# Kernel tuning notes

Measured on AMD Instinct MI355X. Metric: run time of the kernel, lower is better.

The kernel has to match this reference:

```python
import jax, jax.numpy as jnp
import numpy as np

B, H, W, C = 32, 64, 64, 192
WS, SHIFT, NH = 8, 4, 6
HID = int(C * 2.0)
N = WS * WS
HD = C // NH
SCALE = HD ** -0.5


def _rel_index():
    coords = np.stack(np.meshgrid(np.arange(WS), np.arange(WS), indexing='ij')).reshape(2, -1)
    rel = (coords[:, :, None] - coords[:, None, :]).transpose(1, 2, 0)
    rel[:, :, 0] += WS - 1
    rel[:, :, 1] += WS - 1
    rel[:, :, 0] *= 2 * WS - 1
    return rel.sum(-1)  # [N, N] int


def _attn_mask():
    img = np.zeros((H, W))
    cnt = 0
    sl = (slice(0, -WS), slice(-WS, -SHIFT), slice(-SHIFT, None))
    for hs in sl:
        for ws_ in sl:
            img[hs, ws_] = cnt
            cnt += 1
    mw = img.reshape(H // WS, WS, W // WS, WS).transpose(0, 2, 1, 3).reshape(-1, N)
    am = mw[:, None, :] - mw[:, :, None]  # unsqueeze(1) - unsqueeze(2)
    return np.where(am != 0, -100.0, 0.0).astype(np.float32)  # [nW, N, N]

REL_IDX = jnp.asarray(_rel_index())
ATTN_MASK = jnp.asarray(_attn_mask())


def _ln(x, g, b, eps=1e-5):
    m = jnp.mean(x, -1, keepdims=True)
    v = jnp.mean((x - m) ** 2, -1, keepdims=True)
    return (x - m) * jax.lax.rsqrt(v + eps) * g + b


def setup_inputs() -> dict:
    key = jax.random.key(0)
    ks = jax.random.split(key, 16)
    s = 0.02
    return {
        'x': jax.random.normal(ks[0], (B, H, W, C), jnp.float32),
        'norm1_g': jnp.ones((C,), jnp.float32),
        'norm1_b': jnp.zeros((C,), jnp.float32),
        'qkv_w': jax.random.normal(ks[1], (C, 3 * C), jnp.float32) * s,
        'qkv_b': jnp.zeros((3 * C,), jnp.float32),
        'proj_w': jax.random.normal(ks[2], (C, C), jnp.float32) * s,
        'proj_b': jnp.zeros((C,), jnp.float32),
        'rel_bias_table': jax.random.normal(ks[3], ((2 * WS - 1) ** 2, NH), jnp.float32) * s,
        'norm2_g': jnp.ones((C,), jnp.float32),
        'norm2_b': jnp.zeros((C,), jnp.float32),
        'mlp_w1': jax.random.normal(ks[4], (C, HID), jnp.float32) * s,
        'mlp_b1': jnp.zeros((HID,), jnp.float32),
        'mlp_w2': jax.random.normal(ks[5], (HID, C), jnp.float32) * s,
        'mlp_b2': jnp.zeros((C,), jnp.float32),
    }


def reference(x, norm1_g, norm1_b, qkv_w, qkv_b, proj_w, proj_b, rel_bias_table,
              norm2_g, norm2_b, mlp_w1, mlp_b1, mlp_w2, mlp_b2):
    nWh, nWw = H // WS, W // WS
    nW = nWh * nWw
    shortcut = x
    h = _ln(x, norm1_g, norm1_b)
    # cyclic shift
    h = jnp.roll(h, shift=(-SHIFT, -SHIFT), axis=(1, 2))
    # window partition -> [B*nW, N, C]
    hw = h.reshape(B, nWh, WS, nWw, WS, C).transpose(0, 1, 3, 2, 4, 5).reshape(B * nW, N, C)
    # qkv
    qkv = hw @ qkv_w + qkv_b  # [B_, N, 3C]
    qkv = qkv.reshape(B * nW, N, 3, NH, HD).transpose(2, 0, 3, 1, 4)
    q, k, v = qkv[0], qkv[1], qkv[2]  # [B_, NH, N, HD]
    attn = jnp.einsum('bhnd,bhmd->bhnm', q * SCALE, k)
    # relative position bias: [NH, N, N]
    bias = rel_bias_table[REL_IDX.reshape(-1)].reshape(N, N, NH).transpose(2, 0, 1)
    attn = attn + bias[None]
    # shift mask
    attn = attn.reshape(B, nW, NH, N, N) + ATTN_MASK[None, :, None]
    attn = jax.nn.softmax(attn.reshape(B * nW, NH, N, N), axis=-1)
    out = jnp.einsum('bhnm,bhmd->bhnd', attn, v).transpose(0, 2, 1, 3).reshape(B * nW, N, C)
    out = out @ proj_w + proj_b
    # window reverse
    out = out.reshape(B, nWh, nWw, WS, WS, C).transpose(0, 1, 3, 2, 4, 5).reshape(B, H, W, C)
    out = jnp.roll(out, shift=(SHIFT, SHIFT), axis=(1, 2))
    h = shortcut + out
    # MLP
    m = _ln(h, norm2_g, norm2_b)
    m = jax.nn.gelu(m @ mlp_w1 + mlp_b1, approximate=False) @ mlp_w2 + mlp_b2
    return h + m
```

## Files before the change

### kernel.cpp

```cpp
#include <hip/hip_runtime.h>
#include <hip/hip_bf16.h>

#define CC 192

typedef __attribute__((ext_vector_type(8))) short bf16x8;
typedef __attribute__((ext_vector_type(4))) float f32x4;

__device__ __forceinline__ unsigned short f2bf(float f) {
    unsigned int u = __float_as_uint(f);
    u = (u + 0x7fffu + ((u >> 16) & 1u)) >> 16;
    return (unsigned short)u;
}

__device__ __forceinline__ f32x4 mfma16(bf16x8 a, bf16x8 b, f32x4 c) {
    return __builtin_amdgcn_mfma_f32_16x16x32_bf16(a, b, c, 0, 0, 0);
}

__global__ void k_prep(const float* __restrict__ qkv_w, const float* __restrict__ proj_w,
                       const float* __restrict__ w1, const float* __restrict__ w2,
                       const float* __restrict__ relTab,
                       unsigned short* __restrict__ qkvT, unsigned short* __restrict__ projT,
                       unsigned short* __restrict__ w1T, unsigned short* __restrict__ w2T,
                       float* __restrict__ biasT) {
    int idx = blockIdx.x * blockDim.x + threadIdx.x;
    if (idx < 110592) { int n = idx / 192, k = idx % 192; qkvT[idx] = f2bf(qkv_w[k * 576 + n]); return; }
    idx -= 110592;
    if (idx < 36864)  { int n = idx / 192, k = idx % 192; projT[idx] = f2bf(proj_w[k * 192 + n]); return; }
    idx -= 36864;
    if (idx < 73728)  { int n = idx / 192, k = idx % 192; w1T[idx] = f2bf(w1[k * 384 + n]); return; }
    idx -= 73728;
    if (idx < 73728)  { int n = idx / 384, k = idx % 384; w2T[idx] = f2bf(w2[k * 192 + n]); return; }
    idx -= 73728;
    if (idx < 24576) {
        int h = idx >> 12, i = (idx >> 6) & 63, j = idx & 63;
        int yi = i >> 3, xi = i & 7, yj = j >> 3, xj = j & 7;
        int rel = (yi - yj + 7) * 15 + (xi - xj + 7);
        biasT[idx] = relTab[rel * 6 + h];
    }
}

__global__ __launch_bounds__(768, 3) void k_fused(
    const float* __restrict__ x,
    const float* __restrict__ n1g, const float* __restrict__ n1b,
    const unsigned short* __restrict__ qkvT, const float* __restrict__ qkv_b,
    const unsigned short* __restrict__ projT, const float* __restrict__ proj_b,
    const float* __restrict__ biasTab,
    const float* __restrict__ n2g, const float* __restrict__ n2b,
    const unsigned short* __restrict__ w1T, const float* __restrict__ b1,
    const unsigned short* __restrict__ w2T, const float* __restrict__ b2,
    float* __restrict__ out)
{
    __shared__ __align__(16) char smem[73728];
    __shared__ int sOpos[64];
    char* const rA = smem;
    char* const rQ = smem + 24576;
    char* const rK = smem + 49152;
    char* const rG = smem + 24576;

    const int tid = threadIdx.x;
    const int wid = blockIdx.x;
    const int b = wid >> 6;
    const int win = wid & 63;
    const int wh = win >> 3, ww = win & 7;
    const int lane = tid & 63;
    const int wave = tid >> 6;
    const int lhi = lane >> 4, llo = lane & 15;

    if (tid < 512) {
        const int tok = tid >> 3;
        const int ch0 = (tid & 7) * 24;
        const int yi = tok >> 3, xi = tok & 7;
        const int oy = (wh * 8 + yi + 4) & 63;
        const int ox = (ww * 8 + xi + 4) & 63;
        const int base = ((b * 64 + oy) * 64 + ox) * CC;
        if ((tid & 7) == 0) sOpos[tok] = base;
        float v[24];
        float s = 0.f, ss = 0.f;
        #pragma unroll
        for (int i = 0; i < 6; ++i) {
            const float4 f = *(const float4*)(x + base + ch0 + i * 4);
            v[i*4+0]=f.x; v[i*4+1]=f.y; v[i*4+2]=f.z; v[i*4+3]=f.w;
            s  += f.x + f.y + f.z + f.w;
            ss += f.x*f.x + f.y*f.y + f.z*f.z + f.w*f.w;
        }
        s  += __shfl_xor(s, 1);  s  += __shfl_xor(s, 2);  s  += __shfl_xor(s, 4);
        ss += __shfl_xor(ss, 1); ss += __shfl_xor(ss, 2); ss += __shfl_xor(ss, 4);
        const float mean = s * (1.f / 192.f);
        const float rstd = rsqrtf(ss * (1.f / 192.f) - mean * mean + 1e-5f);
        char* aBase = rA + tok * 384;
        const int sw = (tok & 7) << 4;
        #pragma unroll
        for (int i = 0; i < 12; ++i) {
            const int c = ch0 + i * 2;
            const float a0 = (v[i*2+0] - mean) * rstd * n1g[c]   + n1b[c];
            const float a1 = (v[i*2+1] - mean) * rstd * n1g[c+1] + n1b[c+1];
            *(unsigned int*)(aBase + ((c * 2) ^ sw)) =
                (unsigned int)f2bf(a0) | ((unsigned int)f2bf(a1) << 16);
        }
    }
    __syncthreads();

    {
        const int cbase = wave * 48;
        f32x4 acc[4][3] = {};
        #pragma unroll
        for (int ks = 0; ks < 6; ++ks) {
            bf16x8 af[4];
            const int kbyte = ks * 64 + lhi * 16;
            #pragma unroll
            for (int m = 0; m < 4; ++m) {
                const int row = m * 16 + llo;
                af[m] = *(const bf16x8*)(rA + row * 384 + (kbyte ^ ((row & 7) << 4)));
            }
            #pragma unroll
            for (int n = 0; n < 3; ++n) {
                const int col = cbase + n * 16 + llo;
                const bf16x8 bfr = *(const bf16x8*)(qkvT + col * 192 + ks * 32 + lhi * 8);
                #pragma unroll
                for (int m = 0; m < 4; ++m) acc[m][n] = mfma16(af[m], bfr, acc[m][n]);
            }
        }
        __syncthreads();
        #pragma unroll
        for (int n = 0; n < 3; ++n) {
            const int c0 = cbase + n * 16;
            const int which = c0 / 192;
            const int rem = c0 - which * 192;
            const int h = rem >> 5;
            const int d = (rem & 31) + llo;
            const float bia = qkv_b[c0 + llo];
            #pragma unroll
            for (int m = 0; m < 4; ++m) {
                #pragma unroll
                for (int r = 0; r < 4; ++r) {
                    const int row = m * 16 + lhi * 4 + r;
                    if (which == 0)
                        *(unsigned short*)(rQ + h * 4096 + row * 64 + ((2 * d) ^ ((row & 3) << 4)))
                            = f2bf((acc[m][n][r] + bia) * 0.17677669529663687f);
                    else if (which == 1)
                        *(unsigned short*)(rK + h * 4096 + row * 64 + ((2 * d) ^ ((row & 3) << 4)))
                            = f2bf(acc[m][n][r] + bia);
                    else
                        *(unsigned short*)(rA + h * 4096 + d * 128 + ((2 * row) ^ ((d & 7) << 4)))
                            = f2bf(acc[m][n][r] + bia);
                }
            }
        }
    }
    __syncthreads();

    const int h = wave >> 1;
    const int mh = wave & 1;
    f32x4 pacc[2][2] = {};
    float rinv[2][4];
    {
        bf16x8 qf[2], kf[4];
        #pragma unroll
        for (int m = 0; m < 2; ++m) {
            const int t = (mh * 2 + m) * 16 + llo;
            qf[m] = *(const bf16x8*)(rQ + h * 4096 + t * 64 + ((lhi * 16) ^ ((t & 3) << 4)));
        }
        #pragma unroll
        for (int n = 0; n < 4; ++n) {
            const int t = n * 16 + llo;
            kf[n] = *(const bf16x8*)(rK + h * 4096 + t * 64 + ((lhi * 16) ^ ((t & 3) << 4)));
        }
        __syncthreads();

        f32x4 sacc[2][4] = {};
        #pragma unroll
        for (int m = 0; m < 2; ++m)
            #pragma unroll
            for (int n = 0; n < 4; ++n)
                sacc[m][n] = mfma16(qf[m], kf[n], sacc[m][n]);

        const bool eH = (wh == 7), eW = (ww == 7);
        int idj[4];
        #pragma unroll
        for (int n = 0; n < 4; ++n) {
            const int j = n * 16 + llo;
            idj[n] = (eH ? ((j >> 3) >= 4 ? 2 : 1) : 0) * 3 + (eW ? ((j & 7) >= 4 ? 2 : 1) : 0);
        }
        const float* bT = biasTab + h * 4096;
        #pragma unroll
        for (int m = 0; m < 2; ++m) {
            #pragma unroll
            for (int r = 0; r < 4; ++r) {
                const int i = (mh * 2 + m) * 16 + lhi * 4 + r;
                const int idi = (eH ? ((i >> 3) >= 4 ? 2 : 1) : 0) * 3 +
                                (eW ? ((i & 7) >= 4 ? 2 : 1) : 0);
                float sum = 0.f;
                unsigned short pb[4];
                #pragma unroll
                for (int n = 0; n < 4; ++n) {
                    const int j = n * 16 + llo;
                    float e = __expf(sacc[m][n][r] + bT[i * 64 + j]);
                    if (idi != idj[n]) e = 0.f;
                    sum += e;
                    pb[n] = f2bf(e);
                }
                sum += __shfl_xor(sum, 1);
                sum += __shfl_xor(sum, 2);
                sum += __shfl_xor(sum, 4);
                sum += __shfl_xor(sum, 8);
                rinv[m][r] = 1.f / sum;
                #pragma unroll
                for (int n = 0; n < 4; ++n) {
                    const int j = n * 16 + llo;
                    *(unsigned short*)(rQ + h * 8192 + i * 128 + ((2 * j) ^ ((i & 7) << 4))) = pb[n];
                }
            }
        }
        #pragma unroll
        for (int ks = 0; ks < 2; ++ks) {
            bf16x8 pf[2];
            #pragma unroll
            for (int m = 0; m < 2; ++m) {
                const int t = (mh * 2 + m) * 16 + llo;
                pf[m] = *(const bf16x8*)(rQ + h * 8192 + t * 128 + ((ks * 64 + lhi * 16) ^ ((t & 7) << 4)));
            }
            #pragma unroll
            for (int n = 0; n < 2; ++n) {
                const int d = n * 16 + llo;
                const bf16x8 vf = *(const bf16x8*)(rA + h * 4096 + d * 128 + ((ks * 64 + lhi * 16) ^ ((d & 7) << 4)));
                #pragma unroll
                for (int m = 0; m < 2; ++m) pacc[m][n] = mfma16(pf[m], vf, pacc[m][n]);
            }
        }
    }
    __syncthreads();
    {
        #pragma unroll
        for (int m = 0; m < 2; ++m) {
            #pragma unroll
            for (int n = 0; n < 2; ++n) {
                const int c = h * 32 + n * 16 + llo;
                #pragma unroll
                for (int r = 0; r < 4; ++r) {
                    const int i = (mh * 2 + m) * 16 + lhi * 4 + r;
                    *(unsigned short*)(rA + i * 384 + ((c * 2) ^ ((i & 7) << 4)))
                        = f2bf(pacc[m][n][r] * rinv[m][r]);
                }
            }
        }
    }
    __syncthreads();

    {
        const int cbase = wave * 16;
        f32x4 acc[4] = {};
        #pragma unroll
        for (int ks = 0; ks < 6; ++ks) {
            bf16x8 af[4];
            const int kbyte = ks * 64 + lhi * 16;
            #pragma unroll
            for (int m = 0; m < 4; ++m) {
                const int row = m * 16 + llo;
                af[m] = *(const bf16x8*)(rA + row * 384 + (kbyte ^ ((row & 7) << 4)));
            }
            const int col = cbase + llo;
            const bf16x8 bfr = *(const bf16x8*)(projT + col * 192 + ks * 32 + lhi * 8);
            #pragma unroll
            for (int m = 0; m < 4; ++m) acc[m] = mfma16(af[m], bfr, acc[m]);
        }
        const int c = cbase + llo;
        const float pb = proj_b[c];
        #pragma unroll
        for (int m = 0; m < 4; ++m) {
            #pragma unroll
            for (int r = 0; r < 4; ++r) {
                const int i = m * 16 + lhi * 4 + r;
                const int base = sOpos[i];
                out[base + c] = x[base + c] + acc[m][r] + pb;
            }
        }
    }
    __syncthreads();

    if (tid < 512) {
        const int tok = tid >> 3;
        const int ch0 = (tid & 7) * 24;
        const float* hp = out + sOpos[tok];
        float v[24]; float s = 0.f, ss = 0.f;
        #pragma unroll
        for (int i = 0; i < 6; ++i) {
            const float4 f = *(const float4*)(hp + ch0 + i * 4);
            v[i*4]=f.x; v[i*4+1]=f.y; v[i*4+2]=f.z; v[i*4+3]=f.w;
            s += f.x + f.y + f.z + f.w;
            ss += f.x*f.x + f.y*f.y + f.z*f.z + f.w*f.w;
        }
        s  += __shfl_xor(s, 1);  s  += __shfl_xor(s, 2);  s  += __shfl_xor(s, 4);
        ss += __shfl_xor(ss, 1); ss += __shfl_xor(ss, 2); ss += __shfl_xor(ss, 4);
        const float mean = s * (1.f / 192.f);
        const float rstd = rsqrtf(ss * (1.f / 192.f) - mean * mean + 1e-5f);
        char* aBase = rA + tok * 384;
        const int sw = (tok & 7) << 4;
        #pragma unroll
        for (int i = 0; i < 12; ++i) {
            const int c = ch0 + i * 2;
            const float a0 = (v[i*2]   - mean) * rstd * n2g[c]   + n2b[c];
            const float a1 = (v[i*2+1] - mean) * rstd * n2g[c+1] + n2b[c+1];
            *(unsigned int*)(aBase + ((c * 2) ^ sw)) =
                (unsigned int)f2bf(a0) | ((unsigned int)f2bf(a1) << 16);
        }
    }
    __syncthreads();

    {
        const int cbase = wave * 32;
        f32x4 acc[4][2] = {};
        #pragma unroll
        for (int ks = 0; ks < 6; ++ks) {
            bf16x8 af[4];
            const int kbyte = ks * 64 + lhi * 16;
            #pragma unroll
            for (int m = 0; m < 4; ++m) {
                const int row = m * 16 + llo;
                af[m] = *(const bf16x8*)(rA + row * 384 + (kbyte ^ ((row & 7) << 4)));
            }
            #pragma unroll
            for (int n = 0; n < 2; ++n) {
                const int col = cbase + n * 16 + llo;
                const bf16x8 bfr = *(const bf16x8*)(w1T + col * 192 + ks * 32 + lhi * 8);
                #pragma unroll
                for (int m = 0; m < 4; ++m) acc[m][n] = mfma16(af[m], bfr, acc[m][n]);
            }
        }
        #pragma unroll
        for (int n = 0; n < 2; ++n) {
            const int c = cbase + n * 16 + llo;
            const float bb = b1[c];
            #pragma unroll
            for (int m = 0; m < 4; ++m) {
                #pragma unroll
                for (int r = 0; r < 4; ++r) {
                    const int i = m * 16 + lhi * 4 + r;
                    const float u = acc[m][n][r] + bb;
                    const float g = 0.5f * u * (1.f + erff(u * 0.70710678118654752f));
                    *(unsigned short*)(rG + i * 768 + ((c * 2) ^ ((i & 7) << 4))) = f2bf(g);
                }
            }
        }
    }
    __syncthreads();

    {
        const int cbase = wave * 16;
        f32x4 acc[4] = {};
        #pragma unroll
        for (int ks = 0; ks < 12; ++ks) {
            bf16x8 af[4];
            const int kbyte = ks * 64 + lhi * 16;
            #pragma unroll
            for (int m = 0; m < 4; ++m) {
                const int row = m * 16 + llo;
                af[m] = *(const bf16x8*)(rG + row * 768 + (kbyte ^ ((row & 7) << 4)));
            }
            const int col = cbase + llo;
            const bf16x8 bfr = *(const bf16x8*)(w2T + col * 384 + ks * 32 + lhi * 8);
            #pragma unroll
            for (int m = 0; m < 4; ++m) acc[m] = mfma16(af[m], bfr, acc[m]);
        }
        const int c = cbase + llo;
        const float bb = b2[c];
        #pragma unroll
        for (int m = 0; m < 4; ++m) {
            #pragma unroll
            for (int r = 0; r < 4; ++r) {
                const int i = m * 16 + lhi * 4 + r;
                float* p = out + sOpos[i] + c;
                *p = *p + acc[m][r] + bb;
            }
        }
    }
}

extern "C" void kernel_launch(void* const* d_in, const int* in_sizes, int n_in,
                              void* d_out, int out_size, void* d_ws, size_t ws_size,
                              hipStream_t stream)
{
    const float* x      = (const float*)d_in[0];
    const float* n1g    = (const float*)d_in[1];
    const float* n1b    = (const float*)d_in[2];
    const float* qkv_w  = (const float*)d_in[3];
    const float* qkv_b  = (const float*)d_in[4];
    const float* proj_w = (const float*)d_in[5];
    const float* proj_b = (const float*)d_in[6];
    const float* relTab = (const float*)d_in[7];
    const float* n2g    = (const float*)d_in[8];
    const float* n2b    = (const float*)d_in[9];
    const float* w1     = (const float*)d_in[10];
    const float* b1     = (const float*)d_in[11];
    const float* w2     = (const float*)d_in[12];
    const float* b2     = (const float*)d_in[13];
    float* out = (float*)d_out;

    char* ws = (char*)d_ws;
    unsigned short* qkvT  = (unsigned short*)(ws);
    unsigned short* projT = (unsigned short*)(ws + 221184);
    unsigned short* w1T   = (unsigned short*)(ws + 294912);
    unsigned short* w2T   = (unsigned short*)(ws + 442368);
    float*          biasT = (float*)(ws + 589824);

    k_prep<<<1248, 256, 0, stream>>>(qkv_w, proj_w, w1, w2, relTab, qkvT, projT, w1T, w2T, biasT);
    k_fused<<<2048, 768, 0, stream>>>(x, n1g, n1b, qkvT, qkv_b, projT, proj_b, biasT,
                                      n2g, n2b, w1T, b1, w2T, b2, out);
}
```

Measured before the change: 297.0 us.

## Shrink fused Swin block LDS footprint to fit more workgroups per CU

Reorganizes shared-memory use in the fused Swin block kernel so the footprint drops from 72KB to 60KB. V is now staged in two halves, and the MLP is split into two hidden-column chunks that reuse a smaller GELU buffer. The QKV GEMM work is redistributed so each wave holds its own Q/K tile and a slice of V. Launch bounds are raised to 6 blocks per CU to target higher occupancy and better latency hiding. The cost is extra __syncthreads barriers, more live accumulators (accV held across attention) and higher register pressure under the tighter bound.

```diff
diff --git a/kernel.cpp b/kernel.cpp
--- a/kernel.cpp
+++ b/kernel.cpp
@@ -39,7 +39,7 @@
     }
 }
 
-__global__ __launch_bounds__(768, 3) void k_fused(
+__global__ __launch_bounds__(768, 6) void k_fused(
     const float* __restrict__ x,
     const float* __restrict__ n1g, const float* __restrict__ n1b,
     const unsigned short* __restrict__ qkvT, const float* __restrict__ qkv_b,
@@ -50,12 +50,8 @@
     const unsigned short* __restrict__ w2T, const float* __restrict__ b2,
     float* __restrict__ out)
 {
-    __shared__ __align__(16) char smem[73728];
+    __shared__ __align__(16) char smem[61440];
     __shared__ int sOpos[64];
-    char* const rA = smem;
-    char* const rQ = smem + 24576;
-    char* const rK = smem + 49152;
-    char* const rG = smem + 24576;
 
     const int tid = threadIdx.x;
     const int wid = blockIdx.x;
@@ -87,7 +83,7 @@
         ss += __shfl_xor(ss, 1); ss += __shfl_xor(ss, 2); ss += __shfl_xor(ss, 4);
         const float mean = s * (1.f / 192.f);
         const float rstd = rsqrtf(ss * (1.f / 192.f) - mean * mean + 1e-5f);
-        char* aBase = rA + tok * 384;
+        char* aBase = smem + tok * 384;
         const int sw = (tok & 7) << 4;
         #pragma unroll
         for (int i = 0; i < 12; ++i) {
@@ -100,9 +96,12 @@
     }
     __syncthreads();
 
-    {
-        const int cbase = wave * 48;
-        f32x4 acc[4][3] = {};
+    const int w = wave;
+    f32x4 accQK[4][2] = {};
+    f32x4 accV[4] = {};
+    {
+        const int cb = 32 * w;
+        const int cv = 384 + 16 * w;
         #pragma unroll
         for (int ks = 0; ks < 6; ++ks) {
             bf16x8 af[4];
@@ -110,47 +109,55 @@
             #pragma unroll
             for (int m = 0; m < 4; ++m) {
                 const int row = m * 16 + llo;
-                af[m] = *(const bf16x8*)(rA + row * 384 + (kbyte ^ ((row & 7) << 4)));
-            }
-            #pragma unroll
-            for (int n = 0; n < 3; ++n) {
-                const int col = cbase + n * 16 + llo;
-                const bf16x8 bfr = *(const bf16x8*)(qkvT + col * 192 + ks * 32 + lhi * 8);
-                #pragma unroll
-                for (int m = 0; m < 4; ++m) acc[m][n] = mfma16(af[m], bfr, acc[m][n]);
-            }
-        }
-        __syncthreads();
-        #pragma unroll
-        for (int n = 0; n < 3; ++n) {
-            const int c0 = cbase + n * 16;
-            const int which = c0 / 192;
-            const int rem = c0 - which * 192;
-            const int h = rem >> 5;
-            const int d = (rem & 31) + llo;
-            const float bia = qkv_b[c0 + llo];
+                af[m] = *(const bf16x8*)(smem + row * 384 + (kbyte ^ ((row & 7) << 4)));
+            }
+            #pragma unroll
+            for (int n = 0; n < 2; ++n) {
+                const bf16x8 bfr = *(const bf16x8*)(qkvT + (cb + n * 16 + llo) * 192 + ks * 32 + lhi * 8);
+                #pragma unroll
+                for (int m = 0; m < 4; ++m) accQK[m][n] = mfma16(af[m], bfr, accQK[m][n]);
+            }
+            const bf16x8 bfv = *(const bf16x8*)(qkvT + (cv + llo) * 192 + ks * 32 + lhi * 8);
+            #pragma unroll
+            for (int m = 0; m < 4; ++m) accV[m] = mfma16(af[m], bfv, accV[m]);
+        }
+    }
+    __syncthreads();
+
+    {
+        const bool isK = (w >= 6);
+        char* const dst = smem + (isK ? 36864 + (w - 6) * 4096 : 12288 + w * 4096);
+        #pragma unroll
+        for (int n = 0; n < 2; ++n) {
+            const int d = n * 16 + llo;
+            const float bia = qkv_b[32 * w + n * 16 + llo];
             #pragma unroll
             for (int m = 0; m < 4; ++m) {
                 #pragma unroll
                 for (int r = 0; r < 4; ++r) {
                     const int row = m * 16 + lhi * 4 + r;
-                    if (which == 0)
-                        *(unsigned short*)(rQ + h * 4096 + row * 64 + ((2 * d) ^ ((row & 3) << 4)))
-                            = f2bf((acc[m][n][r] + bia) * 0.17677669529663687f);
-                    else if (which == 1)
-                        *(unsigned short*)(rK + h * 4096 + row * 64 + ((2 * d) ^ ((row & 3) << 4)))
-                            = f2bf(acc[m][n][r] + bia);
-                    else
-                        *(unsigned short*)(rA + h * 4096 + d * 128 + ((2 * row) ^ ((d & 7) << 4)))
-                            = f2bf(acc[m][n][r] + bia);
-                }
-            }
-        }
-    }
-    __syncthreads();
-
-    const int h = wave >> 1;
-    const int mh = wave & 1;
+                    float vv = accQK[m][n][r] + bia;
+                    if (!isK) vv *= 0.17677669529663687f;
+                    *(unsigned short*)(dst + row * 64 + ((2 * d) ^ ((row & 3) << 4))) = f2bf(vv);
+                }
+            }
+        }
+        const float bv = qkv_b[384 + 16 * w + llo];
+        const int dl = (w & 1) * 16 + llo;
+        char* const vdst = smem + (w >> 1) * 2048;
+        #pragma unroll
+        for (int m = 0; m < 2; ++m) {
+            #pragma unroll
+            for (int r = 0; r < 4; ++r) {
+                const int k = m * 16 + lhi * 4 + r;
+                *(unsigned short*)(vdst + dl * 64 + ((2 * k) ^ ((dl & 3) << 4))) = f2bf(accV[m][r] + bv);
+            }
+        }
+    }
+    __syncthreads();
+
+    const int h = w >> 1;
+    const int mh = w & 1;
     f32x4 pacc[2][2] = {};
     float rinv[2][4];
     {
@@ -158,12 +165,12 @@
         #pragma unroll
         for (int m = 0; m < 2; ++m) {
             const int t = (mh * 2 + m) * 16 + llo;
-            qf[m] = *(const bf16x8*)(rQ + h * 4096 + t * 64 + ((lhi * 16) ^ ((t & 3) << 4)));
+            qf[m] = *(const bf16x8*)(smem + 12288 + h * 4096 + t * 64 + ((lhi * 16) ^ ((t & 3) << 4)));
         }
         #pragma unroll
         for (int n = 0; n < 4; ++n) {
             const int t = n * 16 + llo;
-            kf[n] = *(const bf16x8*)(rK + h * 4096 + t * 64 + ((lhi * 16) ^ ((t & 3) << 4)));
+            kf[n] = *(const bf16x8*)(smem + 36864 + h * 4096 + t * 64 + ((lhi * 16) ^ ((t & 3) << 4)));
         }
         __syncthreads();
 
@@ -207,25 +214,54 @@
                 #pragma unroll
                 for (int n = 0; n < 4; ++n) {
                     const int j = n * 16 + llo;
-                    *(unsigned short*)(rQ + h * 8192 + i * 128 + ((2 * j) ^ ((i & 7) << 4))) = pb[n];
-                }
-            }
-        }
-        #pragma unroll
-        for (int ks = 0; ks < 2; ++ks) {
+                    *(unsigned short*)(smem + 12288 + h * 8192 + i * 128 + ((2 * j) ^ ((i & 7) << 4))) = pb[n];
+                }
+            }
+        }
+        {
             bf16x8 pf[2];
             #pragma unroll
             for (int m = 0; m < 2; ++m) {
                 const int t = (mh * 2 + m) * 16 + llo;
-                pf[m] = *(const bf16x8*)(rQ + h * 8192 + t * 128 + ((ks * 64 + lhi * 16) ^ ((t & 7) << 4)));
+                pf[m] = *(const bf16x8*)(smem + 12288 + h * 8192 + t * 128 + ((lhi * 16) ^ ((t & 7) << 4)));
             }
             #pragma unroll
             for (int n = 0; n < 2; ++n) {
                 const int d = n * 16 + llo;
-                const bf16x8 vf = *(const bf16x8*)(rA + h * 4096 + d * 128 + ((ks * 64 + lhi * 16) ^ ((d & 7) << 4)));
+                const bf16x8 vf = *(const bf16x8*)(smem + h * 2048 + d * 64 + ((lhi * 16) ^ ((d & 3) << 4)));
                 #pragma unroll
                 for (int m = 0; m < 2; ++m) pacc[m][n] = mfma16(pf[m], vf, pacc[m][n]);
             }
+        }
+    }
+    __syncthreads();
+    {
+        const float bv = qkv_b[384 + 16 * w + llo];
+        const int dl = (w & 1) * 16 + llo;
+        char* const vdst = smem + (w >> 1) * 2048;
+        #pragma unroll
+        for (int m = 0; m < 2; ++m) {
+            #pragma unroll
+            for (int r = 0; r < 4; ++r) {
+                const int k = m * 16 + lhi * 4 + r;
+                *(unsigned short*)(vdst + dl * 64 + ((2 * k) ^ ((dl & 3) << 4))) = f2bf(accV[m + 2][r] + bv);
+            }
+        }
+    }
+    __syncthreads();
+    {
+        bf16x8 pf[2];
+        #pragma unroll
+        for (int m = 0; m < 2; ++m) {
+            const int t = (mh * 2 + m) * 16 + llo;
+            pf[m] = *(const bf16x8*)(smem + 12288 + h * 8192 + t * 128 + ((64 + lhi * 16) ^ ((t & 7) << 4)));
+        }
+        #pragma unroll
+        for (int n = 0; n < 2; ++n) {
+            const int d = n * 16 + llo;
+            const bf16x8 vf = *(const bf16x8*)(smem + h * 2048 + d * 64 + ((lhi * 16) ^ ((d & 3) << 4)));
+            #pragma unroll
+            for (int m = 0; m < 2; ++m) pacc[m][n] = mfma16(pf[m], vf, pacc[m][n]);
         }
     }
     __syncthreads();
@@ -238,7 +274,7 @@
                 #pragma unroll
                 for (int r = 0; r < 4; ++r) {
                     const int i = (mh * 2 + m) * 16 + lhi * 4 + r;
-                    *(unsigned short*)(rA + i * 384 + ((c * 2) ^ ((i & 7) << 4)))
+                    *(unsigned short*)(smem + i * 384 + ((c * 2) ^ ((i & 7) << 4)))
                         = f2bf(pacc[m][n][r] * rinv[m][r]);
                 }
             }
@@ -247,7 +283,6 @@
     __syncthreads();
 
     {
-        const int cbase = wave * 16;
         f32x4 acc[4] = {};
         #pragma unroll
         for (int ks = 0; ks < 6; ++ks) {
@@ -256,14 +291,13 @@
             #pragma unroll
             for (int m = 0; m < 4; ++m) {
                 const int row = m * 16 + llo;
-                af[m] = *(const bf16x8*)(rA + row * 384 + (kbyte ^ ((row & 7) << 4)));
-            }
-            const int col = cbase + llo;
-            const bf16x8 bfr = *(const bf16x8*)(projT + col * 192 + ks * 32 + lhi * 8);
+                af[m] = *(const bf16x8*)(smem + row * 384 + (kbyte ^ ((row & 7) << 4)));
+            }
+            const bf16x8 bfr = *(const bf16x8*)(projT + (16 * w + llo) * 192 + ks * 32 + lhi * 8);
             #pragma unroll
             for (int m = 0; m < 4; ++m) acc[m] = mfma16(af[m], bfr, acc[m]);
         }
-        const int c = cbase + llo;
+        const int c = 16 * w + llo;
         const float pb = proj_b[c];
         #pragma unroll
         for (int m = 0; m < 4; ++m) {
@@ -293,7 +327,7 @@
         ss += __shfl_xor(ss, 1); ss += __shfl_xor(ss, 2); ss += __shfl_xor(ss, 4);
         const float mean = s * (1.f / 192.f);
         const float rstd = rsqrtf(ss * (1.f / 192.f) - mean * mean + 1e-5f);
-        char* aBase = rA + tok * 384;
+        char* aBase = smem + tok * 384;
         const int sw = (tok & 7) << 4;
         #pragma unroll
         for (int i = 0; i < 12; ++i) {
@@ -306,62 +340,57 @@
     }
     __syncthreads();
 
-    {
-        const int cbase = wave * 32;
-        f32x4 acc[4][2] = {};
-        #pragma unroll
-        for (int ks = 0; ks < 6; ++ks) {
-            bf16x8 af[4];
-            const int kbyte = ks * 64 + lhi * 16;
-            #pragma unroll
-            for (int m = 0; m < 4; ++m) {
-                const int row = m * 16 + llo;
-                af[m] = *(const bf16x8*)(rA + row * 384 + (kbyte ^ ((row & 7) << 4)));
-            }
-            #pragma unroll
-            for (int n = 0; n < 2; ++n) {
-                const int col = cbase + n * 16 + llo;
-                const bf16x8 bfr = *(const bf16x8*)(w1T + col * 192 + ks * 32 + lhi * 8);
-                #pragma unroll
-                for (int m = 0; m < 4; ++m) acc[m][n] = mfma16(af[m], bfr, acc[m][n]);
-            }
-        }
-        #pragma unroll
-        for (int n = 0; n < 2; ++n) {
-            const int c = cbase + n * 16 + llo;
-            const float bb = b1[c];
+    f32x4 accM[4] = {};
+    #pragma unroll
+    for (int hh = 0; hh < 2; ++hh) {
+        {
+            f32x4 a1[4] = {};
+            #pragma unroll
+            for (int ks = 0; ks < 6; ++ks) {
+                bf16x8 af[4];
+                const int kbyte = ks * 64 + lhi * 16;
+                #pragma unroll
+                for (int m = 0; m < 4; ++m) {
+                    const int row = m * 16 + llo;
+                    af[m] = *(const bf16x8*)(smem + row * 384 + (kbyte ^ ((row & 7) << 4)));
+                }
+                const bf16x8 bfr = *(const bf16x8*)(w1T + (hh * 192 + 16 * w + llo) * 192 + ks * 32 + lhi * 8);
+                #pragma unroll
+                for (int m = 0; m < 4; ++m) a1[m] = mfma16(af[m], bfr, a1[m]);
+            }
+            const int cl = 16 * w + llo;
+            const float bb = b1[hh * 192 + cl];
             #pragma unroll
             for (int m = 0; m < 4; ++m) {
                 #pragma unroll
                 for (int r = 0; r < 4; ++r) {
                     const int i = m * 16 + lhi * 4 + r;
-                    const float u = acc[m][n][r] + bb;
+                    const float u = a1[m][r] + bb;
                     const float g = 0.5f * u * (1.f + erff(u * 0.70710678118654752f));
-                    *(unsigned short*)(rG + i * 768 + ((c * 2) ^ ((i & 7) << 4))) = f2bf(g);
-                }
-            }
-        }
-    }
-    __syncthreads();
-
-    {
-        const int cbase = wave * 16;
-        f32x4 acc[4] = {};
-        #pragma unroll
-        for (int ks = 0; ks < 12; ++ks) {
-            bf16x8 af[4];
-            const int kbyte = ks * 64 + lhi * 16;
-            #pragma unroll
-            for (int m = 0; m < 4; ++m) {
-                const int row = m * 16 + llo;
-                af[m] = *(const bf16x8*)(rG + row * 768 + (kbyte ^ ((row & 7) << 4)));
-            }
-            const int col = cbase + llo;
-            const bf16x8 bfr = *(const bf16x8*)(w2T + col * 384 + ks * 32 + lhi * 8);
-            #pragma unroll
-            for (int m = 0; m < 4; ++m) acc[m] = mfma16(af[m], bfr, acc[m]);
-        }
-        const int c = cbase + llo;
+                    *(unsigned short*)(smem + 24576 + i * 384 + ((2 * cl) ^ ((i & 7) << 4))) = f2bf(g);
+                }
+            }
+        }
+        __syncthreads();
+        {
+            #pragma unroll
+            for (int ks = 0; ks < 6; ++ks) {
+                bf16x8 af[4];
+                const int kbyte = ks * 64 + lhi * 16;
+                #pragma unroll
+                for (int m = 0; m < 4; ++m) {
+                    const int row = m * 16 + llo;
+                    af[m] = *(const bf16x8*)(smem + 24576 + row * 384 + (kbyte ^ ((row & 7) << 4)));
+                }
+                const bf16x8 bfr = *(const bf16x8*)(w2T + (16 * w + llo) * 384 + hh * 192 + ks * 32 + lhi * 8);
+                #pragma unroll
+                for (int m = 0; m < 4; ++m) accM[m] = mfma16(af[m], bfr, accM[m]);
+            }
+        }
+        __syncthreads();
+    }
+    {
+        const int c = 16 * w + llo;
         const float bb = b2[c];
         #pragma unroll
         for (int m = 0; m < 4; ++m) {
@@ -369,7 +398,7 @@
             for (int r = 0; r < 4; ++r) {
                 const int i = m * 16 + lhi * 4 + r;
                 float* p = out + sOpos[i] + c;
-                *p = *p + acc[m][r] + bb;
+                *p = *p + accM[m][r] + bb;
             }
         }
     }
```

Result: slower. 419.1 us (+41.1%).
